# Kernel tuning notes

Hardware: AMD Instinct MI355X
Metric: run time of the kernel (lower is better)

The kernel has to match this reference:

```python
import jax, jax.numpy as jnp
import numpy as np

B, S, E = 2, 2048, 2048
H, KVH, D = 16, 4, 128
GROUPS = H // KVH
WINDOW = 1024
CAP = 50.0
ROPE_BASE = 10000.0
RMS_EPS = 1e-6
LN_EPS = 1e-5

def setup_inputs() -> dict:
    key = jax.random.key(0)
    ks = jax.random.split(key, 5)
    return {
        "x": jax.random.normal(ks[0], (B, S, E), jnp.float32),
        "Wq": jax.random.normal(ks[1], (E, E), jnp.float32) * (1.0 / np.sqrt(E)),
        "Wk": jax.random.normal(ks[2], (KVH * D, E), jnp.float32) * (1.0 / np.sqrt(E)),
        "Wv": jax.random.normal(ks[3], (KVH * D, E), jnp.float32) * (1.0 / np.sqrt(E)),
        "Wo": jax.random.normal(ks[4], (E, E), jnp.float32) * (1.0 / np.sqrt(E * H)),
        "q_norm_w": jnp.ones((D,), jnp.float32),
        "k_norm_w": jnp.ones((D,), jnp.float32),
        "ln_gamma": jnp.ones((E,), jnp.float32),
        "ln_beta": jnp.zeros((E,), jnp.float32),
    }

def _rmsnorm(t, w):
    # normalize over last (head) dim
    var = jnp.mean(jnp.square(t), axis=-1, keepdims=True)
    return t * jax.lax.rsqrt(var + RMS_EPS) * w

def _rope(t):
    # t: [B, h, S, D]; rotate-half RoPE
    half = D // 2
    inv_freq = 1.0 / (ROPE_BASE ** (jnp.arange(0, D, 2, dtype=jnp.float32) / D))  # [D/2]
    ang = jnp.arange(S, dtype=jnp.float32)[:, None] * inv_freq[None, :]  # [S, D/2]
    cos = jnp.concatenate([jnp.cos(ang), jnp.cos(ang)], axis=-1)  # [S, D]
    sin = jnp.concatenate([jnp.sin(ang), jnp.sin(ang)], axis=-1)
    t1, t2 = t[..., :half], t[..., half:]
    rot = jnp.concatenate([-t2, t1], axis=-1)
    return t * cos + rot * sin

def reference(x, Wq, Wk, Wv, Wo, q_norm_w, k_norm_w, ln_gamma, ln_beta):
    b, s, _ = x.shape
    q = (x @ Wq.T).reshape(b, s, H, D).transpose(0, 2, 1, 3)    # [B,H,S,D]
    k = (x @ Wk.T).reshape(b, s, KVH, D).transpose(0, 2, 1, 3)  # [B,KVH,S,D]
    v = (x @ Wv.T).reshape(b, s, KVH, D).transpose(0, 2, 1, 3)
    # QK-RMSNorm (Gemma/PaLM2 style), then RoPE
    q = _rope(_rmsnorm(q, q_norm_w))
    k = _rope(_rmsnorm(k, k_norm_w))
    # GQA: repeat KV heads to match query heads
    k = jnp.repeat(k, GROUPS, axis=1)  # [B,H,S,D]
    v = jnp.repeat(v, GROUPS, axis=1)
    scores = jnp.einsum('bhqd,bhkd->bhqk', q, k) / jnp.sqrt(jnp.asarray(D, x.dtype))
    # tanh logit softcap (Gemma2)
    scores = CAP * jnp.tanh(scores / CAP)
    # causal + sliding-window mask: attend to j with 0 <= i-j < WINDOW
    i = jnp.arange(s)[:, None]
    j = jnp.arange(s)[None, :]
    mask = (j <= i) & ((i - j) < WINDOW)  # [S,S]
    neg = jnp.finfo(scores.dtype).min
    scores = jnp.where(mask[None, None], scores, neg)
    attn = jax.nn.softmax(scores, axis=-1)
    out = jnp.einsum('bhqk,bhkd->bhqd', attn, v)  # [B,H,S,D]
    out = out.transpose(0, 2, 1, 3).reshape(b, s, E) @ Wo.T
    # residual + LayerNorm (post-norm)
    y = x + out
    mu = jnp.mean(y, axis=-1, keepdims=True)
    var = jnp.var(y, axis=-1, keepdims=True)
    return (y - mu) * jax.lax.rsqrt(var + LN_EPS) * ln_gamma + ln_beta
```

## Files before the change

kernel.cpp:

```cpp
#include <hip/hip_runtime.h>
#include <stdint.h>

typedef __attribute__((ext_vector_type(8))) short short8;
typedef __attribute__((ext_vector_type(4))) float f32x4;
typedef unsigned short u16;
typedef unsigned int u32;

#define NTOK 4096
#define E 2048
#define S 2048
#define NH 16
#define NKVH 4
#define HD 128
#define NQKV 3072

__device__ __forceinline__ float bf2f(u16 u) {
    return __uint_as_float(((u32)u) << 16);
}
__device__ __forceinline__ u16 f2bf(float f) {
    u32 u = __float_as_uint(f);
    u32 r = (u + 0x7fffu + ((u >> 16) & 1u)) >> 16;
    return (u16)r;
}
__device__ __forceinline__ void gload_lds16(const u16* g, u16* l) {
    __builtin_amdgcn_global_load_lds(
        (const __attribute__((address_space(1))) unsigned int*)(g),
        (__attribute__((address_space(3))) unsigned int*)(l), 16, 0, 0);
}

__global__ void cast5(const float* __restrict__ x, const float* __restrict__ wq,
                      const float* __restrict__ wk, const float* __restrict__ wv,
                      const float* __restrict__ wo,
                      u16* __restrict__ xb, u16* __restrict__ wqkvb,
                      u16* __restrict__ wob) {
    int i = blockIdx.x * 256 + threadIdx.x;
    const float* s; u16* d; int rel;
    if (i < 2097152)      { s = x;  d = xb;  rel = i; }
    else if (i < 3145728) { s = wq; d = wqkvb; rel = i - 2097152; }
    else if (i < 3407872) { s = wk; d = wqkvb + 4194304; rel = i - 3145728; }
    else if (i < 3670016) { s = wv; d = wqkvb + 5242880; rel = i - 3407872; }
    else                  { s = wo; d = wob; rel = i - 3670016; }
    float4 v = *(const float4*)(s + (size_t)rel * 4);
    ushort4 o;
    o.x = f2bf(v.x); o.y = f2bf(v.y); o.z = f2bf(v.z); o.w = f2bf(v.w);
    *(ushort4*)(d + (size_t)rel * 4) = o;
}

#define TM 128
#define TN 128
#define BK 64

__global__ __launch_bounds__(256, 3)
void gemm_bt(const u16* __restrict__ A, const u16* __restrict__ Bt, float* __restrict__ C,
             int M, int N, int K) {
    __shared__ u16 As[TM * BK];
    __shared__ u16 Bs[TN * BK];
    const int m0 = blockIdx.y * TM;
    const int n0 = blockIdx.x * TN;
    const int tid = threadIdx.x;
    const int w = tid >> 6, lane = tid & 63;
    const int wm = (w >> 1) * 64, wn = (w & 1) * 64;
    const int lr = lane & 15, quad = lane >> 4;

    f32x4 acc[4][4];
#pragma unroll
    for (int mi = 0; mi < 4; mi++)
#pragma unroll
        for (int ni = 0; ni < 4; ni++)
            acc[mi][ni] = (f32x4){0.f, 0.f, 0.f, 0.f};

    const int srow = w * 8 + (lane >> 3);
    const int scol = (lane & 7) * 8;
    const u16* ga0 = A + (size_t)(m0 + srow) * K + scol;
    const u16* gb0 = Bt + (size_t)(n0 + srow) * K + scol;

    for (int kt = 0; kt < K; kt += BK) {
        __syncthreads();
#pragma unroll
        for (int i = 0; i < 4; i++) {
            gload_lds16(ga0 + (size_t)(i * 32) * K + kt, &As[(w * 8 + i * 32) * BK]);
            gload_lds16(gb0 + (size_t)(i * 32) * K + kt, &Bs[(w * 8 + i * 32) * BK]);
        }
        __syncthreads();
#pragma unroll
        for (int kk = 0; kk < BK; kk += 32) {
            const int ko = kk + quad * 8;
            short8 af[4], bfr[4];
#pragma unroll
            for (int mi = 0; mi < 4; mi++)
                af[mi] = *(const short8*)(&As[(wm + mi * 16 + lr) * BK + ko]);
#pragma unroll
            for (int ni = 0; ni < 4; ni++)
                bfr[ni] = *(const short8*)(&Bs[(wn + ni * 16 + lr) * BK + ko]);
#pragma unroll
            for (int mi = 0; mi < 4; mi++)
#pragma unroll
                for (int ni = 0; ni < 4; ni++)
                    acc[mi][ni] = __builtin_amdgcn_mfma_f32_16x16x32_bf16(
                        af[mi], bfr[ni], acc[mi][ni], 0, 0, 0);
        }
    }
#pragma unroll
    for (int mi = 0; mi < 4; mi++)
#pragma unroll
        for (int ni = 0; ni < 4; ni++) {
            int row = m0 + wm + mi * 16 + quad * 4;
            int col = n0 + wn + ni * 16 + lr;
            f32x4 v = acc[mi][ni];
            C[(size_t)(row + 0) * N + col] = v[0];
            C[(size_t)(row + 1) * N + col] = v[1];
            C[(size_t)(row + 2) * N + col] = v[2];
            C[(size_t)(row + 3) * N + col] = v[3];
        }
}

__global__ __launch_bounds__(256)
void rmsrope2(const float* __restrict__ qkv,
              const float* __restrict__ qw, const float* __restrict__ kw,
              u16* __restrict__ qdst, u16* __restrict__ kdst) {
    int p = blockIdx.x * 4 + (threadIdx.x >> 6);
    int lane = threadIdx.x & 63;
    const float* src; const float* w; u16* dst; int HH;
    if (p < NTOK * NH) { src = qkv; w = qw; dst = qdst; HH = NH; }
    else { p -= NTOK * NH; src = qkv + 2048; w = kw; dst = kdst; HH = NKVH; }
    int n = p / HH;
    int h = p - n * HH;
    int b = n >> 11;
    int s = n & 2047;
    const float* row = src + (size_t)n * NQKV + h * HD;
    float t1 = row[lane];
    float t2 = row[lane + 64];
    float ss = t1 * t1 + t2 * t2;
#pragma unroll
    for (int o = 1; o < 64; o <<= 1) ss += __shfl_xor(ss, o);
    float r = rsqrtf(ss * (1.f / 128.f) + 1e-6f);
    float a1 = t1 * r * w[lane];
    float a2 = t2 * r * w[lane + 64];
    float freq = expf(lane * -0.14391156831212787f);
    float ang = (float)s * freq;
    float sn, cs;
    sincosf(ang, &sn, &cs);
    float o1 = a1 * cs - a2 * sn;
    float o2 = a2 * cs + a1 * sn;
    size_t base = (((size_t)(b * HH + h)) * S + s) * HD;
    dst[base + lane] = f2bf(o1);
    dst[base + 64 + lane] = f2bf(o2);
}

#define LDT 65
__global__ __launch_bounds__(256)
void vtrans(const float* __restrict__ src, u16* __restrict__ dst) {
    __shared__ u16 Ts[128 * LDT];
    const int t = threadIdx.x;
    const int s0 = blockIdx.x * 64;
    const int kh = blockIdx.y;
    const int b = blockIdx.z;
    const float* base = src + ((size_t)(b * S + s0)) * NQKV + 2560 + kh * HD;
#pragma unroll
    for (int i = 0; i < 8; i++) {
        int idx = i * 256 + t;
        int r = idx >> 5, c4 = (idx & 31) * 4;
        float4 v = *(const float4*)(base + (size_t)r * NQKV + c4);
        Ts[(c4 + 0) * LDT + r] = f2bf(v.x);
        Ts[(c4 + 1) * LDT + r] = f2bf(v.y);
        Ts[(c4 + 2) * LDT + r] = f2bf(v.z);
        Ts[(c4 + 3) * LDT + r] = f2bf(v.w);
    }
    __syncthreads();
    u16* obase = dst + ((size_t)(b * NKVH + kh) * HD) * S + s0;
#pragma unroll
    for (int i = 0; i < 4; i++) {
        int idx = i * 256 + t;
        int d = idx >> 3, s8 = (idx & 7) * 8;
        const u16* row = &Ts[d * LDT + s8];
        short8 o;
#pragma unroll
        for (int j = 0; j < 8; j++) o[j] = (short)row[j];
        *(short8*)(obase + (size_t)d * S + s8) = o;
    }
}

#define KSX(key, cb) ((key) * 128 + ((((cb) ^ ((key) & 15))) * 8))
#define VSX(d, cb)   ((d) * 64 + ((((cb) ^ ((d) & 7))) * 8))
#define PSX(row, cb) ((row) * 64 + ((((cb) ^ ((row) & 7))) * 8))
#define QBLK 64

__global__ __launch_bounds__(256, 4)
void attn_mfma(const u16* __restrict__ qa, const u16* __restrict__ ka,
               const u16* __restrict__ vt, u16* __restrict__ out) {
    __shared__ u16 Ks[64 * 128];
    __shared__ u16 Vs[128 * 64];
    __shared__ u16 Ps[64 * 64];
    const int tid = threadIdx.x;
    const int w = tid >> 6, lane = tid & 63;
    const int lr = lane & 15, quad = lane >> 4;
    const int hb = blockIdx.x;
    const int h = hb >> 1, b = hb & 1;
    const int kh = h >> 2;
    const int qt = (int)(gridDim.y - 1) - blockIdx.y;
    const int q0 = qt * QBLK;
    const int qg0 = q0 + w * 16;

    const float KQK = 0.0051006974f;
    const float KP  = -144.26950408889634f;

    short8 qf[4];
    {
        const u16* qrow = qa + (((size_t)(b * NH + h)) * S + qg0 + lr) * HD;
#pragma unroll
        for (int c = 0; c < 4; c++)
            qf[c] = *(const short8*)(qrow + c * 32 + quad * 8);
    }

    f32x4 O[8];
#pragma unroll
    for (int dt = 0; dt < 8; dt++) O[dt] = (f32x4){0.f, 0.f, 0.f, 0.f};
    float l[4] = {0.f, 0.f, 0.f, 0.f};

    const u16* kbase0 = ka + (((size_t)(b * NKVH + kh)) * S) * HD;
    const u16* vtbase0 = vt + ((size_t)(b * NKVH + kh) * HD) * S;

    const int jt0 = (q0 >= 1024) ? (q0 - 1024) : 0;
    const int jtend = q0;
    const int qmin = qg0, qmax = qg0 + 15;

    for (int jt = jt0; jt <= jtend; jt += 64) {
        const u16* kbase = kbase0 + (size_t)jt * HD;
        const u16* vtbase = vtbase0 + jt;
        __syncthreads();
#pragma unroll
        for (int i = 0; i < 4; i++) {
            int idx = i * 256 + tid;
            int key = idx >> 4, cbk = (idx & 15) ^ (key & 15);
            gload_lds16(kbase + (size_t)key * HD + cbk * 8,
                        &Ks[(i * 256 + w * 64) * 8]);
            int dd = idx >> 3, cbv = (idx & 7) ^ (dd & 7);
            gload_lds16(vtbase + (size_t)dd * S + cbv * 8,
                        &Vs[(i * 256 + w * 64) * 8]);
        }
        __syncthreads();

        u16* Pw = &Ps[w * 16 * 64];
        bool any = false;

#pragma unroll
        for (int kt = 0; kt < 4; kt++) {
            const int keymin = jt + kt * 16;
            bool need = (keymin <= qmax) && (keymin + 15 >= qmin - 1023);
            bool full = (keymin + 15 <= qmin) && (keymin >= qmax - 1023);
            if (need) {
                any = true;
                f32x4 a = (f32x4){0.f, 0.f, 0.f, 0.f};
#pragma unroll
                for (int c = 0; c < 4; c++) {
                    short8 kf = *(const short8*)(&Ks[KSX(kt * 16 + lr, 4 * c + quad)]);
                    a = __builtin_amdgcn_mfma_f32_16x16x32_bf16(qf[c], kf, a, 0, 0, 0);
                }
#pragma unroll
                for (int r = 0; r < 4; r++) {
                    float t = __builtin_amdgcn_exp2f(a[r] * KQK);
                    float p = __builtin_amdgcn_exp2f(
                        KP * __builtin_amdgcn_rcpf(t + 1.f));
                    if (!full) {
                        int rel = keymin + lr - (qg0 + quad * 4 + r);
                        bool valid = (rel <= 0) && (rel > -1024);
                        p = valid ? p : 0.f;
                    }
                    l[r] += p;
                    Pw[PSX(quad * 4 + r, kt * 2 + (lr >> 3)) + (lr & 7)] =
                        (u16)(__float_as_uint(p) >> 16);
                }
            } else {
#pragma unroll
                for (int r = 0; r < 4; r++)
                    Pw[PSX(quad * 4 + r, kt * 2 + (lr >> 3)) + (lr & 7)] = 0;
            }
        }

        if (any) {
#pragma unroll
            for (int c2 = 0; c2 < 2; c2++) {
                short8 pf = *(const short8*)(&Pw[PSX(lr, c2 * 4 + quad)]);
#pragma unroll
                for (int dt = 0; dt < 8; dt++) {
                    short8 vf = *(const short8*)(&Vs[VSX(dt * 16 + lr, c2 * 4 + quad)]);
                    O[dt] = __builtin_amdgcn_mfma_f32_16x16x32_bf16(pf, vf, O[dt], 0, 0, 0);
                }
            }
        }
    }

#pragma unroll
    for (int r = 0; r < 4; r++) {
        l[r] += __shfl_xor(l[r], 1);
        l[r] += __shfl_xor(l[r], 2);
        l[r] += __shfl_xor(l[r], 4);
        l[r] += __shfl_xor(l[r], 8);
    }
#pragma unroll
    for (int r = 0; r < 4; r++) {
        float inv = 1.f / l[r];
        u16* orow = out + ((size_t)(b * S + qg0 + quad * 4 + r)) * E + h * HD;
#pragma unroll
        for (int dt = 0; dt < 8; dt++)
            orow[dt * 16 + lr] = f2bf(O[dt][r] * inv);
    }
}

__global__ __launch_bounds__(256)
void ln_kernel(const float* __restrict__ x, const float* __restrict__ pr,
               const float* __restrict__ g, const float* __restrict__ be,
               float* __restrict__ out) {
    int n = blockIdx.x;
    int tid = threadIdx.x;
    const float* xr = x + (size_t)n * E;
    const float* p = pr + (size_t)n * E;
    float y[8];
    float s = 0.f, ss = 0.f;
#pragma unroll
    for (int i = 0; i < 2; i++) {
        float4 a = *(const float4*)(xr + tid * 8 + i * 4);
        float4 b = *(const float4*)(p + tid * 8 + i * 4);
        float v0 = a.x + b.x, v1 = a.y + b.y, v2 = a.z + b.z, v3 = a.w + b.w;
        y[i * 4 + 0] = v0; y[i * 4 + 1] = v1; y[i * 4 + 2] = v2; y[i * 4 + 3] = v3;
        s += v0 + v1 + v2 + v3;
        ss += v0 * v0 + v1 * v1 + v2 * v2 + v3 * v3;
    }
#pragma unroll
    for (int o = 1; o < 64; o <<= 1) {
        s += __shfl_xor(s, o);
        ss += __shfl_xor(ss, o);
    }
    __shared__ float r0[4], r1[4];
    int w = tid >> 6;
    if ((tid & 63) == 0) { r0[w] = s; r1[w] = ss; }
    __syncthreads();
    s = r0[0] + r0[1] + r0[2] + r0[3];
    ss = r1[0] + r1[1] + r1[2] + r1[3];
    float mu = s * (1.f / 2048.f);
    float var = ss * (1.f / 2048.f) - mu * mu;
    float rs = rsqrtf(var + 1e-5f);
    float* orow = out + (size_t)n * E;
#pragma unroll
    for (int i = 0; i < 8; i++) {
        int c = tid * 8 + i;
        orow[c] = (y[i] - mu) * rs * g[c] + be[c];
    }
}

extern "C" void kernel_launch(void* const* d_in, const int* in_sizes, int n_in,
                              void* d_out, int out_size, void* d_ws, size_t ws_size,
                              hipStream_t stream) {
    (void)in_sizes; (void)n_in; (void)out_size; (void)ws_size;
    const float* x   = (const float*)d_in[0];
    const float* Wq  = (const float*)d_in[1];
    const float* Wk  = (const float*)d_in[2];
    const float* Wv  = (const float*)d_in[3];
    const float* Wo  = (const float*)d_in[4];
    const float* qnw = (const float*)d_in[5];
    const float* knw = (const float*)d_in[6];
    const float* lng = (const float*)d_in[7];
    const float* lnb = (const float*)d_in[8];
    float* out = (float*)d_out;

    char* ws = (char*)d_ws;
    size_t off = 0;
    auto alloc = [&](size_t bytes) -> char* {
        char* pp = ws + off;
        off = (off + bytes + 255) & ~(size_t)255;
        return pp;
    };
    u16*  xb     = (u16*)alloc((size_t)NTOK * E * 2);
    u16*  Wqkvb  = (u16*)alloc((size_t)NQKV * E * 2);
    u16*  Wob    = (u16*)alloc((size_t)E * E * 2);
    float* qkvraw= (float*)alloc((size_t)NTOK * NQKV * 4);
    u16*  qaa    = (u16*)alloc((size_t)NTOK * E * 2);
    u16*  kaa    = (u16*)alloc((size_t)NTOK * 512 * 2);
    u16*  vtt    = (u16*)alloc((size_t)NTOK * 512 * 2);
    u16*  attn_o = xb;
    float* proj  = qkvraw;

    cast5<<<dim3(18432), 256, 0, stream>>>(x, Wq, Wk, Wv, Wo, xb, Wqkvb, Wob);

    gemm_bt<<<dim3(NQKV / TN, NTOK / TM), 256, 0, stream>>>(xb, Wqkvb, qkvraw, NTOK, NQKV, E);

    rmsrope2<<<dim3((NTOK * NH + NTOK * NKVH) / 4), 256, 0, stream>>>(
        qkvraw, qnw, knw, qaa, kaa);
    vtrans<<<dim3(S / 64, NKVH, 2), 256, 0, stream>>>(qkvraw, vtt);

    attn_mfma<<<dim3(NH * 2, S / QBLK), 256, 0, stream>>>(qaa, kaa, vtt, attn_o);

    gemm_bt<<<dim3(E / TN, NTOK / TM), 256, 0, stream>>>(attn_o, Wob, proj, NTOK, E, E);

    ln_kernel<<<dim3(NTOK), 256, 0, stream>>>(x, proj, lng, lnb, out);
}
```

Measured before the change: 326.3 us.

## Replace GEMM with 256x256 double-buffered 8-wave pipelined MFMA kernel

Replaces the 128x128 single-buffered bf16 GEMM with a 256x256-tile, 512-thread kernel. It double-buffers LDS and issues global-to-LDS loads for upcoming K tiles interleaved with four MFMA quadrants, using explicit waitcnt, barriers and priority bumps. It also adds an XOR swizzle on LDS addresses to avoid bank conflicts and remaps workgroups so neighbouring tiles land on the same XCD. The aim is to hide memory latency and raise arithmetic intensity in the QKV and output projections, at the cost of more registers, lower occupancy and fewer workgroups (192 and 128 tiles).

```diff
diff --git a/kernel.cpp b/kernel.cpp
--- a/kernel.cpp
+++ b/kernel.cpp
@@ -46,66 +46,177 @@
     *(ushort4*)(d + (size_t)rel * 4) = o;
 }
 
-#define TM 128
-#define TN 128
-#define BK 64
-
-__global__ __launch_bounds__(256, 3)
-void gemm_bt(const u16* __restrict__ A, const u16* __restrict__ Bt, float* __restrict__ C,
-             int M, int N, int K) {
-    __shared__ u16 As[TM * BK];
-    __shared__ u16 Bs[TN * BK];
-    const int m0 = blockIdx.y * TM;
-    const int n0 = blockIdx.x * TN;
+#define LADDR(row, ko) ((row) * 64 + ((ko) ^ (((row) & 7) << 3)))
+
+__device__ __forceinline__ void stageA(u16* lds, const u16* g, int ldsrow0,
+                                       int g0, int g1, int kt, int K, int tid) {
+    const int rr = tid >> 3;
+    const int chunk = (tid & 7) ^ (rr & 7);
+    const int w8 = (tid >> 6) * 8;
+    gload_lds16(g + (size_t)(g0 + rr) * K + kt + chunk * 8,
+                lds + (ldsrow0 + w8) * 64);
+    gload_lds16(g + (size_t)(g1 + rr) * K + kt + chunk * 8,
+                lds + (ldsrow0 + 64 + w8) * 64);
+}
+__device__ __forceinline__ void stageB(u16* lds, const u16* g, int ldsrow0,
+                                       int b0, int b1, int kt, int K, int tid) {
+    const int rr = tid >> 3;
+    const int grow = (rr & 31) | ((rr & 32) << 1);
+    const int chunk = (tid & 7) ^ (rr & 7);
+    const int w8 = (tid >> 6) * 8;
+    gload_lds16(g + (size_t)(b0 + grow) * K + kt + chunk * 8,
+                lds + (ldsrow0 + w8) * 64);
+    gload_lds16(g + (size_t)(b1 + grow) * K + kt + chunk * 8,
+                lds + (ldsrow0 + 64 + w8) * 64);
+}
+
+#define GSB   __builtin_amdgcn_sched_barrier(0)
+#define GBAR  __builtin_amdgcn_s_barrier()
+#define LGKM0 do { asm volatile("s_waitcnt lgkmcnt(0)" ::: "memory"); GSB; } while (0)
+#define MIDBAR do { GSB; GBAR; LGKM0; } while (0)
+#define ENDBAR do { __builtin_amdgcn_s_setprio(0); GSB; GBAR; } while (0)
+
+__global__ __launch_bounds__(512, 2)
+void gemm8p(const u16* __restrict__ A, const u16* __restrict__ Bt,
+            float* __restrict__ C, int M, int N, int K) {
+    __shared__ u16 As[2 * 16384];
+    __shared__ u16 Bs[2 * 16384];
     const int tid = threadIdx.x;
     const int w = tid >> 6, lane = tid & 63;
-    const int wm = (w >> 1) * 64, wn = (w & 1) * 64;
     const int lr = lane & 15, quad = lane >> 4;
-
-    f32x4 acc[4][4];
-#pragma unroll
-    for (int mi = 0; mi < 4; mi++)
+    const int qo = quad * 8;
+    const int wm = (w >> 2) * 128, wn = (w & 3) * 64;
+    const int wmh = (w >> 2) * 64, wnq = (w & 3) * 32;
+
+    const int nbx = N >> 8;
+    int wg = blockIdx.x;
+    {
+        const int nwg = gridDim.x;
+        const int q = nwg >> 3, r = nwg & 7;
+        const int xcd = wg & 7, loc = wg >> 3;
+        wg = (xcd < r ? xcd * (q + 1) : r * (q + 1) + (xcd - r) * q) + loc;
+    }
+    const int n0 = (wg % nbx) << 8;
+    const int m0 = (wg / nbx) << 8;
+
+    const u16* gA = A + (size_t)m0 * K;
+    const u16* gB = Bt + (size_t)n0 * K;
+    const int nt = K >> 6;
+
+    f32x4 acc[8][4];
+#pragma unroll
+    for (int mi = 0; mi < 8; mi++)
 #pragma unroll
         for (int ni = 0; ni < 4; ni++)
             acc[mi][ni] = (f32x4){0.f, 0.f, 0.f, 0.f};
 
-    const int srow = w * 8 + (lane >> 3);
-    const int scol = (lane & 7) * 8;
-    const u16* ga0 = A + (size_t)(m0 + srow) * K + scol;
-    const u16* gb0 = Bt + (size_t)(n0 + srow) * K + scol;
-
-    for (int kt = 0; kt < K; kt += BK) {
-        __syncthreads();
-#pragma unroll
-        for (int i = 0; i < 4; i++) {
-            gload_lds16(ga0 + (size_t)(i * 32) * K + kt, &As[(w * 8 + i * 32) * BK]);
-            gload_lds16(gb0 + (size_t)(i * 32) * K + kt, &Bs[(w * 8 + i * 32) * BK]);
+    short8 alo[4][2], ahi[4][2], blo[2][2], bhi[2][2];
+
+    stageA(As, gA, 0, 0, 128, 0, K, tid);
+    stageB(Bs, gB, 0, 0, 128, 0, K, tid);
+    stageB(Bs, gB, 128, 32, 160, 0, K, tid);
+    stageA(As, gA, 128, 64, 192, 0, K, tid);
+    if (nt > 1) {
+        stageA(As + 16384, gA, 0, 0, 128, 64, K, tid);
+        stageB(Bs + 16384, gB, 0, 0, 128, 64, K, tid);
+        stageB(Bs + 16384, gB, 128, 32, 160, 64, K, tid);
+        asm volatile("s_waitcnt vmcnt(6)" ::: "memory");
+    } else {
+        asm volatile("s_waitcnt vmcnt(0)" ::: "memory");
+    }
+    GSB; GBAR;
+
+    for (int t = 0; t < nt; ++t) {
+        const int pb = t & 1;
+        u16* Ap = As + pb * 16384;
+        u16* Bp = Bs + pb * 16384;
+        u16* An = As + (pb ^ 1) * 16384;
+        const int kt1 = (t + 1) << 6, kt2 = (t + 2) << 6;
+
+#pragma unroll
+        for (int mi = 0; mi < 4; mi++)
+#pragma unroll
+            for (int kk = 0; kk < 2; kk++)
+                alo[mi][kk] = *(const short8*)&Ap[LADDR(wmh + mi * 16 + lr, kk * 32 + qo)];
+#pragma unroll
+        for (int ni = 0; ni < 2; ni++)
+#pragma unroll
+            for (int kk = 0; kk < 2; kk++)
+                blo[ni][kk] = *(const short8*)&Bp[LADDR(wnq + ni * 16 + lr, kk * 32 + qo)];
+        if (t + 1 < nt) stageA(An, gA, 128, 64, 192, kt1, K, tid);
+        MIDBAR;
+        __builtin_amdgcn_s_setprio(1);
+#pragma unroll
+        for (int mi = 0; mi < 4; mi++)
+#pragma unroll
+            for (int ni = 0; ni < 2; ni++)
+#pragma unroll
+                for (int kk = 0; kk < 2; kk++)
+                    acc[mi][ni] = __builtin_amdgcn_mfma_f32_16x16x32_bf16(
+                        alo[mi][kk], blo[ni][kk], acc[mi][ni], 0, 0, 0);
+        ENDBAR;
+
+#pragma unroll
+        for (int ni = 0; ni < 2; ni++)
+#pragma unroll
+            for (int kk = 0; kk < 2; kk++)
+                bhi[ni][kk] = *(const short8*)&Bp[LADDR(128 + wnq + ni * 16 + lr, kk * 32 + qo)];
+        if (t + 2 < nt) stageA(Ap, gA, 0, 0, 128, kt2, K, tid);
+        MIDBAR;
+        __builtin_amdgcn_s_setprio(1);
+#pragma unroll
+        for (int mi = 0; mi < 4; mi++)
+#pragma unroll
+            for (int ni = 0; ni < 2; ni++)
+#pragma unroll
+                for (int kk = 0; kk < 2; kk++)
+                    acc[mi][ni + 2] = __builtin_amdgcn_mfma_f32_16x16x32_bf16(
+                        alo[mi][kk], bhi[ni][kk], acc[mi][ni + 2], 0, 0, 0);
+        ENDBAR;
+
+#pragma unroll
+        for (int mi = 0; mi < 4; mi++)
+#pragma unroll
+            for (int kk = 0; kk < 2; kk++)
+                ahi[mi][kk] = *(const short8*)&Ap[LADDR(128 + wmh + mi * 16 + lr, kk * 32 + qo)];
+        if (t + 2 < nt) stageB(Bp, gB, 0, 0, 128, kt2, K, tid);
+        MIDBAR;
+        __builtin_amdgcn_s_setprio(1);
+#pragma unroll
+        for (int mi = 0; mi < 4; mi++)
+#pragma unroll
+            for (int ni = 0; ni < 2; ni++)
+#pragma unroll
+                for (int kk = 0; kk < 2; kk++)
+                    acc[mi + 4][ni + 2] = __builtin_amdgcn_mfma_f32_16x16x32_bf16(
+                        ahi[mi][kk], bhi[ni][kk], acc[mi + 4][ni + 2], 0, 0, 0);
+        ENDBAR;
+
+        if (t + 2 < nt) stageB(Bp, gB, 128, 32, 160, kt2, K, tid);
+        __builtin_amdgcn_s_setprio(1);
+#pragma unroll
+        for (int mi = 0; mi < 4; mi++)
+#pragma unroll
+            for (int ni = 0; ni < 2; ni++)
+#pragma unroll
+                for (int kk = 0; kk < 2; kk++)
+                    acc[mi + 4][ni] = __builtin_amdgcn_mfma_f32_16x16x32_bf16(
+                        ahi[mi][kk], blo[ni][kk], acc[mi + 4][ni], 0, 0, 0);
+        __builtin_amdgcn_s_setprio(0);
+        if (t + 2 >= nt) {
+            asm volatile("s_waitcnt vmcnt(0)" ::: "memory");
+        } else {
+            asm volatile("s_waitcnt vmcnt(6)" ::: "memory");
         }
-        __syncthreads();
-#pragma unroll
-        for (int kk = 0; kk < BK; kk += 32) {
-            const int ko = kk + quad * 8;
-            short8 af[4], bfr[4];
-#pragma unroll
-            for (int mi = 0; mi < 4; mi++)
-                af[mi] = *(const short8*)(&As[(wm + mi * 16 + lr) * BK + ko]);
-#pragma unroll
-            for (int ni = 0; ni < 4; ni++)
-                bfr[ni] = *(const short8*)(&Bs[(wn + ni * 16 + lr) * BK + ko]);
-#pragma unroll
-            for (int mi = 0; mi < 4; mi++)
-#pragma unroll
-                for (int ni = 0; ni < 4; ni++)
-                    acc[mi][ni] = __builtin_amdgcn_mfma_f32_16x16x32_bf16(
-                        af[mi], bfr[ni], acc[mi][ni], 0, 0, 0);
-        }
-    }
-#pragma unroll
-    for (int mi = 0; mi < 4; mi++)
+        GSB; GBAR;
+    }
+
+#pragma unroll
+    for (int mi = 0; mi < 8; mi++)
 #pragma unroll
         for (int ni = 0; ni < 4; ni++) {
-            int row = m0 + wm + mi * 16 + quad * 4;
-            int col = n0 + wn + ni * 16 + lr;
+            const int row = m0 + wm + mi * 16 + quad * 4;
+            const int col = n0 + wn + ni * 16 + lr;
             f32x4 v = acc[mi][ni];
             C[(size_t)(row + 0) * N + col] = v[0];
             C[(size_t)(row + 1) * N + col] = v[1];
@@ -382,7 +493,8 @@
 
     cast5<<<dim3(18432), 256, 0, stream>>>(x, Wq, Wk, Wv, Wo, xb, Wqkvb, Wob);
 
-    gemm_bt<<<dim3(NQKV / TN, NTOK / TM), 256, 0, stream>>>(xb, Wqkvb, qkvraw, NTOK, NQKV, E);
+    gemm8p<<<dim3((NTOK / 256) * (NQKV / 256)), 512, 0, stream>>>(
+        xb, Wqkvb, qkvraw, NTOK, NQKV, E);
 
     rmsrope2<<<dim3((NTOK * NH + NTOK * NKVH) / 4), 256, 0, stream>>>(
         qkvraw, qnw, knw, qaa, kaa);
@@ -390,7 +502,8 @@
 
     attn_mfma<<<dim3(NH * 2, S / QBLK), 256, 0, stream>>>(qaa, kaa, vtt, attn_o);
 
-    gemm_bt<<<dim3(E / TN, NTOK / TM), 256, 0, stream>>>(attn_o, Wob, proj, NTOK, E, E);
+    gemm8p<<<dim3((NTOK / 256) * (E / 256)), 512, 0, stream>>>(
+        attn_o, Wob, proj, NTOK, E, E);
 
     ln_kernel<<<dim3(NTOK), 256, 0, stream>>>(x, proj, lng, lnb, out);
 }
```

After: 339.6 us. +4.1%, slower.
